# Kernel optimization log

Measured on AMD Instinct MI355X. Metric: run time of the kernel, lower is better.

Reference implementation:

```python
import jax, jax.numpy as jnp
import numpy as np

CONTEXT_SIZE = 256  # hardcoded in source; scale = context_size**-0.5, not head_size
EMBED_DIM = 384
HEAD_SIZE = 64
BATCH = 512
SEQ = 256


def setup_inputs() -> dict:
    key = jax.random.key(0)
    ks = jax.random.split(key, 7)
    s = 1.0 / np.sqrt(EMBED_DIM)
    return {
        "x": jax.random.normal(ks[0], (BATCH, SEQ, EMBED_DIM), jnp.float32),
        "Wq": jax.random.uniform(ks[1], (EMBED_DIM, HEAD_SIZE), jnp.float32, -s, s),
        "bq": jax.random.uniform(ks[2], (HEAD_SIZE,), jnp.float32, -s, s),
        "Wk": jax.random.uniform(ks[3], (EMBED_DIM, HEAD_SIZE), jnp.float32, -s, s),
        "bk": jax.random.uniform(ks[4], (HEAD_SIZE,), jnp.float32, -s, s),
        "Wv": jax.random.uniform(ks[5], (EMBED_DIM, HEAD_SIZE), jnp.float32, -s, s),
        "bv": jax.random.uniform(ks[6], (HEAD_SIZE,), jnp.float32, -s, s),
    }


def reference(x, Wq, bq, Wk, bk, Wv, bv):
    # x: [B, T, D]
    T = x.shape[1]
    q = x @ Wq + bq          # [B, T, H]
    k = x @ Wk + bk          # [B, T, H]
    v = x @ Wv + bv          # [B, T, H]
    scale = CONTEXT_SIZE ** (-0.5)  # faithful: source scales by context_size, not head_size
    scores = jnp.einsum("bth,bsh->bts", q, k) * scale  # [B, T, T]
    causal = jnp.tril(jnp.ones((T, T), dtype=bool))
    scores = jnp.where(causal, scores, -jnp.inf)
    attn = jax.nn.softmax(scores, axis=-1)
    # dropout omitted (eval mode / deterministic reference)
    return jnp.einsum("bts,bsh->bth", attn, v)  # [B, T, H]
```

## Files before the change

kernel.cpp:

```cpp
#include <hip/hip_runtime.h>
#include <hip/hip_bf16.h>
#include <stdint.h>

#define B_ 512
#define T_ 256
#define D_ 384
#define H_ 64

typedef __attribute__((ext_vector_type(8))) short bf16x8;
typedef __attribute__((ext_vector_type(4))) float f32x4;
typedef __attribute__((ext_vector_type(16))) float f32x16;

__device__ __forceinline__ unsigned short f2bf(float f) {
  union { float f; unsigned int u; } a; a.f = f;
  unsigned int r = (a.u + 0x7FFFu + ((a.u >> 16) & 1u)) >> 16;
  return (unsigned short)r;
}

__device__ __forceinline__ unsigned int pkbf(float lo, float hi) {
  unsigned int r;
  asm("v_cvt_pk_bf16_f32 %0, %1, %2" : "=v"(r) : "v"(lo), "v"(hi));
  return r;
}

__global__ void prep_wt(const float* __restrict__ Wq, const float* __restrict__ Wk,
                        const float* __restrict__ Wv, unsigned short* __restrict__ wt) {
  int idx = blockIdx.x * 256 + threadIdx.x;
  if (idx >= 192 * 384) return;
  int n = idx / 384, k = idx - n * 384;
  int sel = n >> 6, c = n & 63;
  const float* W = (sel == 0) ? Wq : ((sel == 1) ? Wk : Wv);
  wt[idx] = f2bf(W[k * 64 + c]);
}

__global__ __launch_bounds__(1024) void attn_fused(
    const float* __restrict__ x, const float* __restrict__ bq,
    const float* __restrict__ bk, const float* __restrict__ bv,
    const unsigned short* __restrict__ wt, float* __restrict__ out) {
  extern __shared__ char smem[];
  const int tid = threadIdx.x;
  const int b = blockIdx.x;
  const int wv = tid >> 6, lane = tid & 63;
  const int lo4 = lane & 15, hi4 = lane >> 4;
  const int lo5 = lane & 31, hi5 = lane >> 5;

  const float* xb = x + (size_t)b * T_ * D_;
  const int row0 = 16 * wv + lo4;

  f32x4 acc[12];
#pragma unroll
  for (int ct = 0; ct < 12; ++ct) acc[ct] = (f32x4)0.0f;

  float4 xsA[2], xsB[2];
  {
    const float* p = xb + row0 * D_ + 8 * hi4;
    xsA[0] = *reinterpret_cast<const float4*>(p);
    xsA[1] = *reinterpret_cast<const float4*>(p + 4);
  }

  for (int half = 0; half < 2; ++half) {
#pragma unroll
    for (int i = 0; i < 5; ++i) {
      int u = tid + 1024 * i;
      if (u < 4608) {
        int n = u / 24;
        int mp = u - n * 24;
        int m = mp ^ (n & 7);
        const uint4* src = reinterpret_cast<const uint4*>(wt + n * 384 + half * 192 + 8 * m);
        *reinterpret_cast<uint4*>(smem + 16 * u) = *src;
      }
    }
    __syncthreads();
#pragma unroll
    for (int ks6 = 0; ks6 < 6; ++ks6) {
      int g = 6 * half + ks6;
      float4* cur = ((g & 1) == 0) ? xsA : xsB;
      float4* nxt = ((g & 1) == 0) ? xsB : xsA;
      if (g < 11) {
        const float* p = xb + row0 * D_ + 32 * (g + 1) + 8 * hi4;
        nxt[0] = *reinterpret_cast<const float4*>(p);
        nxt[1] = *reinterpret_cast<const float4*>(p + 4);
      }
      union { bf16x8 v; unsigned int w[4]; } A;
      A.w[0] = pkbf(cur[0].x, cur[0].y); A.w[1] = pkbf(cur[0].z, cur[0].w);
      A.w[2] = pkbf(cur[1].x, cur[1].y); A.w[3] = pkbf(cur[1].z, cur[1].w);
      bf16x8 afr = A.v;
#pragma unroll
      for (int ct = 0; ct < 12; ++ct) {
        int n = 16 * ct + lo4;
        int kbyte = (64 * ks6 + 16 * hi4) ^ ((n & 7) << 4);
        bf16x8 bw = *reinterpret_cast<const bf16x8*>(smem + n * 384 + kbyte);
        acc[ct] = __builtin_amdgcn_mfma_f32_16x16x32_bf16(afr, bw, acc[ct], 0, 0, 0);
      }
    }
    __syncthreads();
  }

#pragma unroll
  for (int ct = 0; ct < 12; ++ct) {
    int n = 16 * ct + lo4;
    float bias = (ct < 4) ? bq[n] : ((ct < 8) ? bk[n - 64] : bv[n - 128]);
    int rowb = 16 * wv + 4 * hi4;
#pragma unroll
    for (int r = 0; r < 4; ++r) {
      int row = rowb + r;
      unsigned short v = f2bf(acc[ct][r] + bias);
      if (ct < 4) {
        int h = n;
        *reinterpret_cast<unsigned short*>(smem + row * 128 + ((2 * h) ^ ((row & 7) << 4))) = v;
      } else if (ct < 8) {
        int h = n - 64;
        *reinterpret_cast<unsigned short*>(smem + 32768 + row * 128 + ((2 * h) ^ ((row & 7) << 4))) = v;
      } else {
        int h = n - 128;
        *reinterpret_cast<unsigned short*>(smem + 65536 + h * 512 + ((2 * row) ^ ((h & 7) << 4))) = v;
      }
    }
  }
  __syncthreads();

  if (wv < 8) {
    const float cexp = 0.09016844005555897f;

    bf16x8 qf[4];
    {
      int row = 32 * wv + lo5;
#pragma unroll
      for (int s = 0; s < 4; ++s)
        qf[s] = *reinterpret_cast<const bf16x8*>(
            smem + row * 128 + (((32 * s + 16 * hi5)) ^ ((row & 7) << 4)));
    }

    f32x16 o0 = (f32x16)0.0f, o1 = (f32x16)0.0f;
    float lsum = 0.0f;

    for (int kb = 0; kb <= wv; ++kb) {
      f32x16 st = (f32x16)0.0f;
      {
        int row = 32 * kb + lo5;
#pragma unroll
        for (int s = 0; s < 4; ++s) {
          bf16x8 kf = *reinterpret_cast<const bf16x8*>(
              smem + 32768 + row * 128 + (((32 * s + 16 * hi5)) ^ ((row & 7) << 4)));
          st = __builtin_amdgcn_mfma_f32_32x32x16_bf16(kf, qf[s], st, 0, 0, 0);
        }
      }
      float p[16];
#pragma unroll
      for (int r = 0; r < 16; ++r) {
        float e = exp2f(cexp * st[r]);
        if (kb == wv) {
          int keyl = (r & 3) + 8 * (r >> 2) + 4 * hi5;
          if (keyl > lo5) e = 0.0f;
        }
        p[r] = e;
        lsum += e;
      }

      union { bf16x8 v; unsigned int w[4]; } A0, A1;
      {
        unsigned int X0 = pkbf(p[0], p[1]),  X1 = pkbf(p[2], p[3]);
        unsigned int Y0 = pkbf(p[4], p[5]),  Y1 = pkbf(p[6], p[7]);
        unsigned int X0p = (unsigned int)__shfl_xor((int)X0, 32);
        unsigned int X1p = (unsigned int)__shfl_xor((int)X1, 32);
        unsigned int Y0p = (unsigned int)__shfl_xor((int)Y0, 32);
        unsigned int Y1p = (unsigned int)__shfl_xor((int)Y1, 32);
        A0.w[0] = hi5 ? Y0p : X0;
        A0.w[1] = hi5 ? Y1p : X1;
        A0.w[2] = hi5 ? Y0  : X0p;
        A0.w[3] = hi5 ? Y1  : X1p;
        unsigned int Z0 = pkbf(p[8], p[9]),   Z1 = pkbf(p[10], p[11]);
        unsigned int W0 = pkbf(p[12], p[13]), W1 = pkbf(p[14], p[15]);
        unsigned int Z0p = (unsigned int)__shfl_xor((int)Z0, 32);
        unsigned int Z1p = (unsigned int)__shfl_xor((int)Z1, 32);
        unsigned int W0p = (unsigned int)__shfl_xor((int)W0, 32);
        unsigned int W1p = (unsigned int)__shfl_xor((int)W1, 32);
        A1.w[0] = hi5 ? W0p : Z0;
        A1.w[1] = hi5 ? W1p : Z1;
        A1.w[2] = hi5 ? W0  : Z0p;
        A1.w[3] = hi5 ? W1  : Z1p;
      }
#pragma unroll
      for (int s2 = 0; s2 < 2; ++s2) {
        bf16x8 pa = s2 ? A1.v : A0.v;
        int kk = 32 * kb + 16 * s2 + 8 * hi5;
#pragma unroll
        for (int ht = 0; ht < 2; ++ht) {
          int h = 32 * ht + lo5;
          bf16x8 vf = *reinterpret_cast<const bf16x8*>(
              smem + 65536 + h * 512 + (((2 * kk)) ^ ((h & 7) << 4)));
          if (ht == 0) o0 = __builtin_amdgcn_mfma_f32_32x32x16_bf16(pa, vf, o0, 0, 0, 0);
          else         o1 = __builtin_amdgcn_mfma_f32_32x32x16_bf16(pa, vf, o1, 0, 0, 0);
        }
      }
    }

    lsum += __shfl_xor(lsum, 32);
    float inv = 1.0f / lsum;
    float* ob = out + (size_t)b * T_ * H_;
#pragma unroll
    for (int r = 0; r < 16; ++r) {
      int ridx = (r & 3) + 8 * (r >> 2) + 4 * hi5;
      float invr = __shfl(inv, ridx);
      int row = 32 * wv + ridx;
      ob[row * H_ + lo5]      = o0[r] * invr;
      ob[row * H_ + 32 + lo5] = o1[r] * invr;
    }
  }
}

extern "C" void kernel_launch(void* const* d_in, const int* in_sizes, int n_in,
                              void* d_out, int out_size, void* d_ws, size_t ws_size,
                              hipStream_t stream) {
  const float* x  = (const float*)d_in[0];
  const float* Wq = (const float*)d_in[1];
  const float* bq = (const float*)d_in[2];
  const float* Wk = (const float*)d_in[3];
  const float* bk = (const float*)d_in[4];
  const float* Wv = (const float*)d_in[5];
  const float* bv = (const float*)d_in[6];
  unsigned short* wt = (unsigned short*)d_ws;
  float* out = (float*)d_out;

  prep_wt<<<288, 256, 0, stream>>>(Wq, Wk, Wv, wt);
  attn_fused<<<B_, 1024, 98304, stream>>>(x, bq, bk, bv, wt, out);
}
```

Baseline: 62.87 us.

## Split causal key blocks across all 16 waves and reduce partials in LDS

Instead of leaving waves 8-15 idle during attention, each query block's key range is split in half. Waves 0-7 take the first half and waves 8-15 the second. The upper waves write their unnormalized partial outputs and row sums to shared memory, and the lower waves add them before normalizing and storing. This is meant to cut the attention-phase critical path, which was set by wave 7 doing all 8 key blocks, at the cost of two extra barriers and an LDS reduction.

```diff
diff --git a/kernel.cpp b/kernel.cpp
--- a/kernel.cpp
+++ b/kernel.cpp
@@ -119,90 +119,119 @@
   }
   __syncthreads();
 
+  const float cexp = 0.09016844005555897f;
+  const int qq = wv & 7;
+  const int half_h = (qq + 2) >> 1;
+  const int kb_begin = (wv < 8) ? 0 : half_h;
+  const int kb_end   = (wv < 8) ? half_h : (qq + 1);
+
+  bf16x8 qf[4];
+  {
+    int row = 32 * qq + lo5;
+#pragma unroll
+    for (int s = 0; s < 4; ++s)
+      qf[s] = *reinterpret_cast<const bf16x8*>(
+          smem + row * 128 + (((32 * s + 16 * hi5)) ^ ((row & 7) << 4)));
+  }
+
+  f32x16 o0 = (f32x16)0.0f, o1 = (f32x16)0.0f;
+  float lsum = 0.0f;
+
+  for (int kb = kb_begin; kb < kb_end; ++kb) {
+    f32x16 st = (f32x16)0.0f;
+    {
+      int row = 32 * kb + lo5;
+#pragma unroll
+      for (int s = 0; s < 4; ++s) {
+        bf16x8 kf = *reinterpret_cast<const bf16x8*>(
+            smem + 32768 + row * 128 + (((32 * s + 16 * hi5)) ^ ((row & 7) << 4)));
+        st = __builtin_amdgcn_mfma_f32_32x32x16_bf16(kf, qf[s], st, 0, 0, 0);
+      }
+    }
+    float p[16];
+#pragma unroll
+    for (int r = 0; r < 16; ++r) {
+      float e = exp2f(cexp * st[r]);
+      if (kb == qq) {
+        int keyl = (r & 3) + 8 * (r >> 2) + 4 * hi5;
+        if (keyl > lo5) e = 0.0f;
+      }
+      p[r] = e;
+      lsum += e;
+    }
+
+    union { bf16x8 v; unsigned int w[4]; } A0, A1;
+    {
+      unsigned int X0 = pkbf(p[0], p[1]),  X1 = pkbf(p[2], p[3]);
+      unsigned int Y0 = pkbf(p[4], p[5]),  Y1 = pkbf(p[6], p[7]);
+      unsigned int X0p = (unsigned int)__shfl_xor((int)X0, 32);
+      unsigned int X1p = (unsigned int)__shfl_xor((int)X1, 32);
+      unsigned int Y0p = (unsigned int)__shfl_xor((int)Y0, 32);
+      unsigned int Y1p = (unsigned int)__shfl_xor((int)Y1, 32);
+      A0.w[0] = hi5 ? Y0p : X0;
+      A0.w[1] = hi5 ? Y1p : X1;
+      A0.w[2] = hi5 ? Y0  : X0p;
+      A0.w[3] = hi5 ? Y1  : X1p;
+      unsigned int Z0 = pkbf(p[8], p[9]),   Z1 = pkbf(p[10], p[11]);
+      unsigned int W0 = pkbf(p[12], p[13]), W1 = pkbf(p[14], p[15]);
+      unsigned int Z0p = (unsigned int)__shfl_xor((int)Z0, 32);
+      unsigned int Z1p = (unsigned int)__shfl_xor((int)Z1, 32);
+      unsigned int W0p = (unsigned int)__shfl_xor((int)W0, 32);
+      unsigned int W1p = (unsigned int)__shfl_xor((int)W1, 32);
+      A1.w[0] = hi5 ? W0p : Z0;
+      A1.w[1] = hi5 ? W1p : Z1;
+      A1.w[2] = hi5 ? W0  : Z0p;
+      A1.w[3] = hi5 ? W1  : Z1p;
+    }
+#pragma unroll
+    for (int s2 = 0; s2 < 2; ++s2) {
+      bf16x8 pa = s2 ? A1.v : A0.v;
+      int kk = 32 * kb + 16 * s2 + 8 * hi5;
+#pragma unroll
+      for (int ht = 0; ht < 2; ++ht) {
+        int h = 32 * ht + lo5;
+        bf16x8 vf = *reinterpret_cast<const bf16x8*>(
+            smem + 65536 + h * 512 + (((2 * kk)) ^ ((h & 7) << 4)));
+        if (ht == 0) o0 = __builtin_amdgcn_mfma_f32_32x32x16_bf16(pa, vf, o0, 0, 0, 0);
+        else         o1 = __builtin_amdgcn_mfma_f32_32x32x16_bf16(pa, vf, o1, 0, 0, 0);
+      }
+    }
+  }
+
+  lsum += __shfl_xor(lsum, 32);
+
+  __syncthreads();
+
+  if (wv >= 8) {
+    char* pbase = smem + 8192 * qq;
+#pragma unroll
+    for (int r = 0; r < 16; ++r) {
+      int ridx = (r & 3) + 8 * (r >> 2) + 4 * hi5;
+      *reinterpret_cast<float*>(pbase + ridx * 256 + 4 * lo5)       = o0[r];
+      *reinterpret_cast<float*>(pbase + ridx * 256 + 128 + 4 * lo5) = o1[r];
+    }
+    if (hi5 == 0)
+      *reinterpret_cast<float*>(smem + 65536 + 128 * qq + 4 * lo5) = lsum;
+  }
+  __syncthreads();
+
   if (wv < 8) {
-    const float cexp = 0.09016844005555897f;
-
-    bf16x8 qf[4];
-    {
-      int row = 32 * wv + lo5;
-#pragma unroll
-      for (int s = 0; s < 4; ++s)
-        qf[s] = *reinterpret_cast<const bf16x8*>(
-            smem + row * 128 + (((32 * s + 16 * hi5)) ^ ((row & 7) << 4)));
-    }
-
-    f32x16 o0 = (f32x16)0.0f, o1 = (f32x16)0.0f;
-    float lsum = 0.0f;
-
-    for (int kb = 0; kb <= wv; ++kb) {
-      f32x16 st = (f32x16)0.0f;
-      {
-        int row = 32 * kb + lo5;
-#pragma unroll
-        for (int s = 0; s < 4; ++s) {
-          bf16x8 kf = *reinterpret_cast<const bf16x8*>(
-              smem + 32768 + row * 128 + (((32 * s + 16 * hi5)) ^ ((row & 7) << 4)));
-          st = __builtin_amdgcn_mfma_f32_32x32x16_bf16(kf, qf[s], st, 0, 0, 0);
-        }
-      }
-      float p[16];
-#pragma unroll
-      for (int r = 0; r < 16; ++r) {
-        float e = exp2f(cexp * st[r]);
-        if (kb == wv) {
-          int keyl = (r & 3) + 8 * (r >> 2) + 4 * hi5;
-          if (keyl > lo5) e = 0.0f;
-        }
-        p[r] = e;
-        lsum += e;
-      }
-
-      union { bf16x8 v; unsigned int w[4]; } A0, A1;
-      {
-        unsigned int X0 = pkbf(p[0], p[1]),  X1 = pkbf(p[2], p[3]);
-        unsigned int Y0 = pkbf(p[4], p[5]),  Y1 = pkbf(p[6], p[7]);
-        unsigned int X0p = (unsigned int)__shfl_xor((int)X0, 32);
-        unsigned int X1p = (unsigned int)__shfl_xor((int)X1, 32);
-        unsigned int Y0p = (unsigned int)__shfl_xor((int)Y0, 32);
-        unsigned int Y1p = (unsigned int)__shfl_xor((int)Y1, 32);
-        A0.w[0] = hi5 ? Y0p : X0;
-        A0.w[1] = hi5 ? Y1p : X1;
-        A0.w[2] = hi5 ? Y0  : X0p;
-        A0.w[3] = hi5 ? Y1  : X1p;
-        unsigned int Z0 = pkbf(p[8], p[9]),   Z1 = pkbf(p[10], p[11]);
-        unsigned int W0 = pkbf(p[12], p[13]), W1 = pkbf(p[14], p[15]);
-        unsigned int Z0p = (unsigned int)__shfl_xor((int)Z0, 32);
-        unsigned int Z1p = (unsigned int)__shfl_xor((int)Z1, 32);
-        unsigned int W0p = (unsigned int)__shfl_xor((int)W0, 32);
-        unsigned int W1p = (unsigned int)__shfl_xor((int)W1, 32);
-        A1.w[0] = hi5 ? W0p : Z0;
-        A1.w[1] = hi5 ? W1p : Z1;
-        A1.w[2] = hi5 ? W0  : Z0p;
-        A1.w[3] = hi5 ? W1  : Z1p;
-      }
-#pragma unroll
-      for (int s2 = 0; s2 < 2; ++s2) {
-        bf16x8 pa = s2 ? A1.v : A0.v;
-        int kk = 32 * kb + 16 * s2 + 8 * hi5;
-#pragma unroll
-        for (int ht = 0; ht < 2; ++ht) {
-          int h = 32 * ht + lo5;
-          bf16x8 vf = *reinterpret_cast<const bf16x8*>(
-              smem + 65536 + h * 512 + (((2 * kk)) ^ ((h & 7) << 4)));
-          if (ht == 0) o0 = __builtin_amdgcn_mfma_f32_32x32x16_bf16(pa, vf, o0, 0, 0, 0);
-          else         o1 = __builtin_amdgcn_mfma_f32_32x32x16_bf16(pa, vf, o1, 0, 0, 0);
-        }
-      }
-    }
-
-    lsum += __shfl_xor(lsum, 32);
+    char* pbase = smem + 8192 * qq;
+#pragma unroll
+    for (int r = 0; r < 16; ++r) {
+      int ridx = (r & 3) + 8 * (r >> 2) + 4 * hi5;
+      o0[r] += *reinterpret_cast<const float*>(pbase + ridx * 256 + 4 * lo5);
+      o1[r] += *reinterpret_cast<const float*>(pbase + ridx * 256 + 128 + 4 * lo5);
+    }
+    lsum += *reinterpret_cast<const float*>(smem + 65536 + 128 * qq + 4 * lo5);
+
     float inv = 1.0f / lsum;
     float* ob = out + (size_t)b * T_ * H_;
 #pragma unroll
     for (int r = 0; r < 16; ++r) {
       int ridx = (r & 3) + 8 * (r >> 2) + 4 * hi5;
       float invr = __shfl(inv, ridx);
-      int row = 32 * wv + ridx;
+      int row = 32 * qq + ridx;
       ob[row * H_ + lo5]      = o0[r] * invr;
       ob[row * H_ + 32 + lo5] = o1[r] * invr;
     }
```

Result: slower. 64.38 us (+2.4%).
